# Optimization experiments

Hardware: AMD Instinct MI355X
Metric: run time of the kernel (lower is better)

## Reference

```python
import jax, jax.numpy as jnp
import numpy as np

B, T, D = 4, 2048, 1024
H, Dh = 16, 64


def setup_inputs() -> dict:
    key = jax.random.key(0)
    ks = jax.random.split(key, 5)
    # kaiming_normal_ on [H, Dh, D]: fan_in = Dh*D (torch default fan_in over dims[1:]),
    # std = sqrt(2/fan_in); exact init distribution does not affect correctness checks.
    std_qkv = float(np.sqrt(2.0 / (Dh * D)))
    std_o = float(np.sqrt(2.0 / (D * Dh)))
    return {
        "x": jax.random.normal(ks[0], (B, T, D), dtype=jnp.float32),
        "W_Q": jax.random.normal(ks[1], (H, Dh, D), dtype=jnp.float32) * std_qkv,
        "b_Q": jnp.zeros((H, Dh), dtype=jnp.float32),
        "W_K": jax.random.normal(ks[2], (H, Dh, D), dtype=jnp.float32) * std_qkv,
        "b_K": jnp.zeros((H, Dh), dtype=jnp.float32),
        "W_V": jax.random.normal(ks[3], (H, Dh, D), dtype=jnp.float32) * std_qkv,
        "b_V": jnp.zeros((H, Dh), dtype=jnp.float32),
        "W_O": jax.random.normal(ks[4], (H, D, Dh), dtype=jnp.float32) * std_o,
        "b_O": jnp.zeros((D,), dtype=jnp.float32),
    }


def reference(x, W_Q, b_Q, W_K, b_K, W_V, b_V, W_O, b_O):
    # Q/K/V: [batch, tok, heads, d_head]
    Q = jnp.einsum("btd,hkd->bthk", x, W_Q) + b_Q
    K = jnp.einsum("btd,hkd->bthk", x, W_K) + b_K
    V = jnp.einsum("btd,hkd->bthk", x, W_V) + b_V
    d_head = W_Q.shape[1]
    # scores: [batch, heads, tok_Q, tok_K]
    scores = jnp.einsum("bqhk,bshk->bhqs", Q, K) / jnp.sqrt(jnp.asarray(d_head, x.dtype))
    attn = jax.nn.softmax(scores, axis=-1)
    # out per head: [batch, tok_Q, heads, d_head]
    out_h = jnp.einsum("bhqs,bshk->bqhk", attn, V)
    # project back: [batch, tok, d_model]
    return jnp.einsum("bqhk,hdk->bqd", out_h, W_O) + b_O
```

## Files before the change

kernel.cpp:

```cpp
#include <hip/hip_runtime.h>
#include <stdint.h>


typedef __attribute__((ext_vector_type(8))) short bf16x8;
typedef __attribute__((ext_vector_type(4))) float f32x4;

#define MFMA32 __builtin_amdgcn_mfma_f32_16x16x32_bf16

#if __has_builtin(__builtin_amdgcn_exp2f)
#define EXP2(x) __builtin_amdgcn_exp2f(x)
#else
#define EXP2(x) exp2f(x)
#endif

__device__ __forceinline__ unsigned short f2bf(float f) {
  union { float f; unsigned int u; } v; v.f = f;
  unsigned int r = v.u + 0x7FFFu + ((v.u >> 16) & 1u);
  return (unsigned short)(r >> 16);
}

__device__ __forceinline__ void gl_lds16(const void* g, void* l) {
  __builtin_amdgcn_global_load_lds(
      (const __attribute__((address_space(1))) unsigned int*)g,
      (__attribute__((address_space(3))) unsigned int*)l, 16, 0, 0);
}

__device__ __forceinline__ unsigned packbf2(float lo, float hi) {
  union { float f; unsigned u; } a, b; a.f = lo; b.f = hi;
  return __builtin_amdgcn_perm(b.u, a.u, 0x07060302u);
}

__device__ __forceinline__ int rho(int r) { return (r & 3) | ((r >> 1) & 4); }

__device__ __forceinline__ void conv8(const float* __restrict__ src,
                                      unsigned short* __restrict__ dst, int i) {
  const float4* sp = (const float4*)src;
  float4 a = sp[2 * i], b = sp[2 * i + 1];
  union { unsigned short u[8]; uint4 v; } o;
  o.u[0] = f2bf(a.x); o.u[1] = f2bf(a.y); o.u[2] = f2bf(a.z); o.u[3] = f2bf(a.w);
  o.u[4] = f2bf(b.x); o.u[5] = f2bf(b.y); o.u[6] = f2bf(b.z); o.u[7] = f2bf(b.w);
  ((uint4*)dst)[i] = o.v;
}

__global__ __launch_bounds__(256) void prep_all(
    const float* __restrict__ x, const float* __restrict__ WQ,
    const float* __restrict__ WK, const float* __restrict__ WV,
    const float* __restrict__ WO, unsigned short* __restrict__ Xb,
    unsigned short* __restrict__ Wqkv, unsigned short* __restrict__ Wot) {
  const int bx = blockIdx.x, t = threadIdx.x;
  if (bx < 4096) {
    conv8(x, Xb, bx * 256 + t);
  } else if (bx < 4608) {
    conv8(WQ, Wqkv, (bx - 4096) * 256 + t);
  } else if (bx < 5120) {
    conv8(WK, Wqkv + 1048576, (bx - 4608) * 256 + t);
  } else if (bx < 5632) {
    conv8(WV, Wqkv + 2097152, (bx - 5120) * 256 + t);
  } else {
    int tid = (bx - 5632) * 256 + t;
    int h = tid >> 13, rem = tid & 8191;
    int d = rem >> 3, c = rem & 7;
    const float4* sp = (const float4*)(WO + (size_t)h * 65536 + d * 64 + c * 8);
    float4 a = sp[0], e = sp[1];
    union { unsigned short u[8]; uint4 v; } o;
    o.u[0] = f2bf(a.x); o.u[1] = f2bf(a.y); o.u[2] = f2bf(a.z); o.u[3] = f2bf(a.w);
    o.u[4] = f2bf(e.x); o.u[5] = f2bf(e.y); o.u[6] = f2bf(e.z); o.u[7] = f2bf(e.w);
    *(uint4*)(Wot + (size_t)d * 1024 + h * 64 + c * 8) = o.v;
  }
}


template <int MH, int C>
__device__ __forceinline__ void qkv_ds_a(const unsigned short* A, int wm, int quad,
                                         int l15, bf16x8 ar[4][2]) {
#pragma unroll
  for (int ii = 0; ii < 4; ++ii) {
    int ra = wm * 128 + MH * 64 + ii * 16 + l15;
    ar[ii][C] = *(const bf16x8*)(A + ra * 64 + (((C * 4 + quad) ^ (ra & 7)) * 8));
  }
}

template <int C>
__device__ __forceinline__ void qkv_ds_b(const unsigned short* B, int wn, int quad,
                                         int l15, bf16x8 br[3][2]) {
#pragma unroll
  for (int nj = 0; nj < 3; ++nj) {
    int rb = wn * 48 + nj * 16 + l15;
    br[nj][C] = *(const bf16x8*)(B + rb * 64 + (((C * 4 + quad) ^ (rb & 7)) * 8));
  }
}

template <int MH, int C>
__device__ __forceinline__ void qkv_mf(const bf16x8 ar[4][2], const bf16x8 br[3][2],
                                       f32x4 acc[8][3]) {
#pragma unroll
  for (int ii = 0; ii < 4; ++ii)
#pragma unroll
    for (int nj = 0; nj < 3; ++nj)
      acc[MH * 4 + ii][nj] =
          MFMA32(ar[ii][C], br[nj][C], acc[MH * 4 + ii][nj], 0, 0, 0);
}

#define QKV_BAR() __builtin_amdgcn_s_barrier()
#define QKV_LGKM0() asm volatile("s_waitcnt lgkmcnt(0)" ::: "memory")
#define SA_(bb, kt, u) \
  gl_lds16(Xb + (size_t)aoff[u] + (size_t)(kt) * 64, lds + (bb)*28672 + adst[u])
#define SB_(bb, kt, u) \
  gl_lds16(Wqkv + (size_t)boff[u] + (size_t)(kt) * 64, lds + (bb)*28672 + 16384 + bdst[u])

__global__ __launch_bounds__(512, 2) void gemm_qkv(
    const unsigned short* __restrict__ Xb, const unsigned short* __restrict__ Wqkv,
    const float* __restrict__ bQ, const float* __restrict__ bK,
    const float* __restrict__ bV, unsigned short* __restrict__ Qg,
    unsigned short* __restrict__ Kg, unsigned int* __restrict__ Vpg) {
  __shared__ unsigned short lds[57344];
  const int tid = threadIdx.x, lane = tid & 63, w = tid >> 6;
  const int quad = lane >> 4, l15 = lane & 15;
  const int wm = w >> 2, wn = w & 3;
  const int m0 = blockIdx.x * 256, n0 = blockIdx.y * 192;

  int aoff[4], adst[4];
#pragma unroll
  for (int u = 0; u < 4; ++u) {
    int s = u * 512 + tid, row = s >> 3;
    aoff[u] = (m0 + row) * 1024 + (((s & 7) ^ (row & 7)) * 8);
    adst[u] = s * 8;
  }
  int boff[3], bdst[3];
#pragma unroll
  for (int u = 0; u < 3; ++u) {
    int s = u * 512 + tid, row = s >> 3;
    boff[u] = (n0 + row) * 1024 + (((s & 7) ^ (row & 7)) * 8);
    bdst[u] = s * 8;
  }

  const unsigned short* A0 = lds;
  const unsigned short* B0 = lds + 16384;
  const unsigned short* A1 = lds + 28672;
  const unsigned short* B1 = lds + 45056;

  f32x4 acc[8][3];
#pragma unroll
  for (int i = 0; i < 8; ++i)
#pragma unroll
    for (int j = 0; j < 3; ++j) acc[i][j] = (f32x4){0.f, 0.f, 0.f, 0.f};
  bf16x8 ar[4][2], br[3][2];

  SA_(0, 0, 0); SA_(0, 0, 1); SA_(0, 0, 2); SA_(0, 0, 3);
  SB_(0, 0, 0); SB_(0, 0, 1); SB_(0, 0, 2);
  SB_(1, 1, 0); SB_(1, 1, 1); SB_(1, 1, 2);
  asm volatile("s_waitcnt vmcnt(3)" ::: "memory");
  QKV_BAR();

#pragma unroll 1
  for (int i = 0; i < 8; ++i) {
    const int tn = 2 * i + 2;
    const bool st = (i < 7);
    qkv_ds_a<0, 0>(A0, wm, quad, l15, ar);
    qkv_ds_b<0>(B0, wn, quad, l15, br);
    SA_(1, 2 * i + 1, 0); SA_(1, 2 * i + 1, 1);
    QKV_BAR(); QKV_LGKM0();
    __builtin_amdgcn_s_setprio(1); qkv_mf<0, 0>(ar, br, acc); __builtin_amdgcn_s_setprio(0);
    QKV_BAR();
    qkv_ds_a<0, 1>(A0, wm, quad, l15, ar);
    qkv_ds_b<1>(B0, wn, quad, l15, br);
    SA_(1, 2 * i + 1, 2); SA_(1, 2 * i + 1, 3);
    QKV_BAR(); QKV_LGKM0();
    __builtin_amdgcn_s_setprio(1); qkv_mf<0, 1>(ar, br, acc); __builtin_amdgcn_s_setprio(0);
    QKV_BAR();
    qkv_ds_a<1, 0>(A0, wm, quad, l15, ar);
    if (st) { SB_(0, tn, 0); SB_(0, tn, 1); }
    QKV_BAR(); QKV_LGKM0();
    __builtin_amdgcn_s_setprio(1); qkv_mf<1, 0>(ar, br, acc); __builtin_amdgcn_s_setprio(0);
    QKV_BAR();
    qkv_ds_a<1, 1>(A0, wm, quad, l15, ar);
    if (st) SB_(0, tn, 2);
    QKV_BAR(); QKV_LGKM0();
    __builtin_amdgcn_s_setprio(1); qkv_mf<1, 1>(ar, br, acc); __builtin_amdgcn_s_setprio(0);
    if (st) asm volatile("s_waitcnt vmcnt(3)" ::: "memory");
    else    asm volatile("s_waitcnt vmcnt(0)" ::: "memory");
    QKV_BAR();
    qkv_ds_a<0, 0>(A1, wm, quad, l15, ar);
    qkv_ds_b<0>(B1, wn, quad, l15, br);
    if (st) { SA_(0, tn, 0); SA_(0, tn, 1); }
    QKV_BAR(); QKV_LGKM0();
    __builtin_amdgcn_s_setprio(1); qkv_mf<0, 0>(ar, br, acc); __builtin_amdgcn_s_setprio(0);
    QKV_BAR();
    qkv_ds_a<0, 1>(A1, wm, quad, l15, ar);
    qkv_ds_b<1>(B1, wn, quad, l15, br);
    if (st) { SA_(0, tn, 2); SA_(0, tn, 3); }
    QKV_BAR(); QKV_LGKM0();
    __builtin_amdgcn_s_setprio(1); qkv_mf<0, 1>(ar, br, acc); __builtin_amdgcn_s_setprio(0);
    QKV_BAR();
    qkv_ds_a<1, 0>(A1, wm, quad, l15, ar);
    if (st) { SB_(1, tn + 1, 0); SB_(1, tn + 1, 1); }
    QKV_BAR(); QKV_LGKM0();
    __builtin_amdgcn_s_setprio(1); qkv_mf<1, 0>(ar, br, acc); __builtin_amdgcn_s_setprio(0);
    QKV_BAR();
    qkv_ds_a<1, 1>(A1, wm, quad, l15, ar);
    if (st) SB_(1, tn + 1, 2);
    QKV_BAR(); QKV_LGKM0();
    __builtin_amdgcn_s_setprio(1); qkv_mf<1, 1>(ar, br, acc); __builtin_amdgcn_s_setprio(0);
    asm volatile("s_waitcnt vmcnt(3)" ::: "memory");
    QKV_BAR();
  }

#pragma unroll
  for (int nj = 0; nj < 3; ++nj) {
    const int n_abs = n0 + wn * 48 + nj * 16 + l15;
    const int type = n_abs >> 10;
    const int n_in = n_abs & 1023;
    const int h = n_in >> 6, kh = n_in & 63;
    const float bv = ((type == 0) ? bQ : (type == 1) ? bK : bV)[n_in];
#pragma unroll
    for (int mi = 0; mi < 8; ++mi) {
      const int mb = m0 + wm * 128 + mi * 16 + quad * 4;
      const int b = mb >> 11, tb = mb & 2047;
      if (type == 2) {
        uint2 pk;
        pk.x = (unsigned)f2bf(acc[mi][nj][0] + bv) |
               ((unsigned)f2bf(acc[mi][nj][1] + bv) << 16);
        pk.y = (unsigned)f2bf(acc[mi][nj][2] + bv) |
               ((unsigned)f2bf(acc[mi][nj][3] + bv) << 16);
        *(uint2*)(Vpg + ((size_t)(b * 16 + h) * 64 + kh) * 1024 + (tb >> 1)) = pk;
      } else {
        unsigned short* dst =
            ((type == 0) ? Qg : Kg) + ((size_t)(b * 16 + h) * 2048 + tb) * 64 + kh;
        const float sc = (type == 0) ? 0.18033688011112042f : 1.0f;
        dst[0]   = f2bf((acc[mi][nj][0] + bv) * sc);
        dst[64]  = f2bf((acc[mi][nj][1] + bv) * sc);
        dst[128] = f2bf((acc[mi][nj][2] + bv) * sc);
        dst[192] = f2bf((acc[mi][nj][3] + bv) * sc);
      }
    }
  }
}

#undef SA_
#undef SB_
#undef QKV_BAR
#undef QKV_LGKM0

__device__ __forceinline__ void stage_kv(const unsigned short* __restrict__ Kb,
                                         const unsigned int* __restrict__ Vb,
                                         unsigned short* smem, int tid, int s0, int b) {
#pragma unroll
  for (int u = 0; u < 2; ++u) {
    int s = u * 256 + tid, row = s >> 3, g = (s & 7) ^ rho(row);
    gl_lds16(Kb + (size_t)(s0 + row) * 64 + g * 8, smem + b * 8192 + s * 8);
    gl_lds16(Vb + (size_t)row * 1024 + (s0 >> 1) + g * 4,
             smem + b * 8192 + 4096 + s * 8);
  }
}

__global__ __launch_bounds__(256, 2) void flash_attn(
    const unsigned short* __restrict__ Qg, const unsigned short* __restrict__ Kg,
    const unsigned int* __restrict__ Vpg, unsigned short* __restrict__ OH) {
  __shared__ unsigned short smem[16384];
  const int tid = threadIdx.x, lane = tid & 63, w = tid >> 6;
  const int quad = lane >> 4, l15 = lane & 15;
  const int bh = blockIdx.x, qt = blockIdx.y;

  const unsigned short* Qb = Qg + ((size_t)bh * 2048 + qt * 256) * 64;
  const unsigned short* Kb = Kg + (size_t)bh * 2048 * 64;
  const unsigned int*  Vb = Vpg + (size_t)bh * 64 * 1024;

#pragma unroll
  for (int u = 0; u < 8; ++u) {
    int s = u * 256 + tid, row = s >> 3;
    gl_lds16(Qb + row * 64 + ((s & 7) ^ (row & 7)) * 8, smem + s * 8);
  }
  __syncthreads();

  bf16x8 qf[4][2];
#pragma unroll
  for (int qi = 0; qi < 4; ++qi) {
    int row = w * 64 + qi * 16 + l15;
#pragma unroll
    for (int c = 0; c < 2; ++c)
      qf[qi][c] = *(const bf16x8*)(smem + row * 64 + (((c * 4 + quad) ^ (row & 7)) * 8));
  }
  __syncthreads();

  stage_kv(Kb, Vb, smem, tid, 0, 0);

  f32x4 o[4][4];
  float l_part[4] = {0.f, 0.f, 0.f, 0.f};
#pragma unroll
  for (int qi = 0; qi < 4; ++qi)
#pragma unroll
    for (int nj = 0; nj < 4; ++nj) o[qi][nj] = (f32x4){0.f, 0.f, 0.f, 0.f};

  for (int t = 0; t < 32; ++t) {
    __syncthreads();
    if (t < 31) stage_kv(Kb, Vb, smem, tid, (t + 1) * 64, (t + 1) & 1);
    const unsigned short* Kd = smem + (t & 1) * 8192;
    const unsigned short* Vd = Kd + 4096;

#pragma unroll
    for (int blk = 0; blk < 2; ++blk) {
      bf16x8 vb[4];
#pragma unroll
      for (int nj = 0; nj < 4; ++nj) {
        int vrow = nj * 16 + l15;
        vb[nj] = *(const bf16x8*)(Vd + vrow * 64 + (((blk * 4 + quad) ^ rho(vrow)) * 8));
      }
      union { unsigned u[4]; bf16x8 v; } pa[4];
#pragma unroll
      for (int v = 0; v < 2; ++v) {
        int krow = blk * 32 + 8 * (l15 >> 2) + 4 * v + (l15 & 3);
        const unsigned short* kr = Kd + krow * 64;
        bf16x8 ka0 = *(const bf16x8*)(kr + ((quad ^ rho(krow)) * 8));
        bf16x8 ka1 = *(const bf16x8*)(kr + (((4 + quad) ^ rho(krow)) * 8));
#pragma unroll
        for (int qi = 0; qi < 4; ++qi) {
          f32x4 S = (f32x4){0.f, 0.f, 0.f, 0.f};
          S = MFMA32(ka0, qf[qi][0], S, 0, 0, 0);
          S = MFMA32(ka1, qf[qi][1], S, 0, 0, 0);
          float e0 = EXP2(S[0]), e1 = EXP2(S[1]), e2 = EXP2(S[2]), e3 = EXP2(S[3]);
          l_part[qi] += (e0 + e1) + (e2 + e3);
          pa[qi].u[2 * v] = packbf2(e0, e1);
          pa[qi].u[2 * v + 1] = packbf2(e2, e3);
        }
      }
#pragma unroll
      for (int nj = 0; nj < 4; ++nj)
#pragma unroll
        for (int qi = 0; qi < 4; ++qi)
          o[qi][nj] = MFMA32(pa[qi].v, vb[nj], o[qi][nj], 0, 0, 0);
    }
  }

  const int b = bh >> 4, h = bh & 15;
#pragma unroll
  for (int qi = 0; qi < 4; ++qi) {
    float l = l_part[qi];
    l += __shfl_xor(l, 16);
    l += __shfl_xor(l, 32);
    float linv = 1.0f / l;
#pragma unroll
    for (int r = 0; r < 4; ++r) {
      float lr = __shfl(linv, 4 * quad + r);
      int trow = qt * 256 + w * 64 + qi * 16 + 4 * quad + r;
#pragma unroll
      for (int nj = 0; nj < 4; ++nj) {
        int col = h * 64 + nj * 16 + l15;
        OH[((size_t)b * 2048 + trow) * 1024 + col] = f2bf(o[qi][nj][r] * lr);
      }
    }
  }
}

__global__ __launch_bounds__(256) void gemm_o(
    const unsigned short* __restrict__ OHm, const unsigned short* __restrict__ Wot,
    const float* __restrict__ bO, float* __restrict__ Out) {
  __shared__ unsigned short As[128 * 64];
  __shared__ unsigned short Bs[64 * 64];
  const int tid = threadIdx.x, lane = tid & 63, w = tid >> 6;
  const int quad = lane >> 4, l15 = lane & 15;
  const int wm = w & 1, wn = w >> 1;
  const int m0 = blockIdx.x * 128, n0 = blockIdx.y * 64;
  f32x4 acc[4][2];
#pragma unroll
  for (int i = 0; i < 4; ++i)
#pragma unroll
    for (int j = 0; j < 2; ++j) acc[i][j] = (f32x4){0.f, 0.f, 0.f, 0.f};

  for (int k0 = 0; k0 < 1024; k0 += 64) {
    __syncthreads();
#pragma unroll
    for (int u = 0; u < 4; ++u) {
      int s = u * 256 + tid, row = s >> 3;
      int cl = ((s & 7) ^ (row & 7)) * 8;
      gl_lds16(OHm + (size_t)(m0 + row) * 1024 + k0 + cl, As + s * 8);
    }
#pragma unroll
    for (int u = 0; u < 2; ++u) {
      int s = u * 256 + tid, row = s >> 3;
      int cl = ((s & 7) ^ (row & 7)) * 8;
      gl_lds16(Wot + (size_t)(n0 + row) * 1024 + k0 + cl, Bs + s * 8);
    }
    __syncthreads();
    bf16x8 af[4][2], bfr[2][2];
#pragma unroll
    for (int i = 0; i < 4; ++i) {
      int ra = wm * 64 + i * 16 + l15;
#pragma unroll
      for (int c = 0; c < 2; ++c)
        af[i][c] = *(const bf16x8*)(As + ra * 64 + (((c * 4 + quad) ^ (ra & 7)) * 8));
    }
#pragma unroll
    for (int j = 0; j < 2; ++j) {
      int rb = wn * 32 + j * 16 + l15;
#pragma unroll
      for (int c = 0; c < 2; ++c)
        bfr[j][c] = *(const bf16x8*)(Bs + rb * 64 + (((c * 4 + quad) ^ (rb & 7)) * 8));
    }
#pragma unroll
    for (int mi = 0; mi < 4; ++mi)
#pragma unroll
      for (int nj = 0; nj < 2; ++nj) {
        acc[mi][nj] = MFMA32(af[mi][0], bfr[nj][0], acc[mi][nj], 0, 0, 0);
        acc[mi][nj] = MFMA32(af[mi][1], bfr[nj][1], acc[mi][nj], 0, 0, 0);
      }
  }

#pragma unroll
  for (int nj = 0; nj < 2; ++nj) {
    const int n = n0 + wn * 32 + nj * 16 + l15;
    const float bv = bO[n];
#pragma unroll
    for (int mi = 0; mi < 4; ++mi) {
      const int mb = m0 + wm * 64 + mi * 16 + quad * 4;
#pragma unroll
      for (int r = 0; r < 4; ++r)
        Out[(size_t)(mb + r) * 1024 + n] = acc[mi][nj][r] + bv;
    }
  }
}

extern "C" void kernel_launch(void* const* d_in, const int* in_sizes, int n_in,
                              void* d_out, int out_size, void* d_ws, size_t ws_size,
                              hipStream_t stream) {
  const float* x  = (const float*)d_in[0];
  const float* WQ = (const float*)d_in[1];
  const float* bQ = (const float*)d_in[2];
  const float* WK = (const float*)d_in[3];
  const float* bK = (const float*)d_in[4];
  const float* WV = (const float*)d_in[5];
  const float* bV = (const float*)d_in[6];
  const float* WO = (const float*)d_in[7];
  const float* bO = (const float*)d_in[8];
  float* out = (float*)d_out;

  char* ws = (char*)d_ws;
  unsigned short* Xb   = (unsigned short*)(ws);
  unsigned short* OH   = (unsigned short*)(ws);
  unsigned short* Wqkv = (unsigned short*)(ws + 16777216);
  unsigned short* Wot  = (unsigned short*)(ws + 23068672);
  unsigned short* Qg   = (unsigned short*)(ws + 25165824);
  unsigned short* Kg   = (unsigned short*)(ws + 41943040);
  unsigned int*   Vpg  = (unsigned int*)  (ws + 58720256);

  prep_all<<<6144, 256, 0, stream>>>(x, WQ, WK, WV, WO, Xb, Wqkv, Wot);

  dim3 g1(32, 16);
  gemm_qkv<<<g1, 512, 0, stream>>>(Xb, Wqkv, bQ, bK, bV, Qg, Kg, Vpg);
  dim3 g2(64, 8);
  flash_attn<<<g2, 256, 0, stream>>>(Qg, Kg, Vpg, OH);
  dim3 g3(64, 16);
  gemm_o<<<g3, 256, 0, stream>>>(OH, Wot, bO, out);
}
```

Baseline: 252.9 us.

## Enlarge output-projection GEMM tile to 128x128 and remap block order for locality

New measurement: 258.0 us. 1.02x slower.

```diff
diff --git a/kernel.cpp b/kernel.cpp
--- a/kernel.cpp
+++ b/kernel.cpp
@@ -69,6 +69,50 @@
   }
 }
 
+__device__ __forceinline__ void gemm_mainloop_1024(
+    const unsigned short* __restrict__ A, const unsigned short* __restrict__ B,
+    unsigned short* As, unsigned short* Bs, int m0, int n0, f32x4 acc[4][4]) {
+  const int tid = threadIdx.x;
+  const int lane = tid & 63, w = tid >> 6;
+  const int quad = lane >> 4, l15 = lane & 15;
+  const int wm = w & 1, wn = w >> 1;
+  int srow[4], scl[4];
+#pragma unroll
+  for (int u = 0; u < 4; ++u) {
+    int s = u * 256 + tid;
+    srow[u] = s >> 3;
+    scl[u] = ((s & 7) ^ ((s >> 3) & 7)) * 8;
+  }
+  for (int k0 = 0; k0 < 1024; k0 += 64) {
+    __syncthreads();
+#pragma unroll
+    for (int u = 0; u < 4; ++u) {
+      int s = u * 256 + tid;
+      gl_lds16(A + (size_t)(m0 + srow[u]) * 1024 + k0 + scl[u], As + s * 8);
+      gl_lds16(B + (size_t)(n0 + srow[u]) * 1024 + k0 + scl[u], Bs + s * 8);
+    }
+    __syncthreads();
+    bf16x8 af[4][2], bfr[4][2];
+#pragma unroll
+    for (int i = 0; i < 4; ++i) {
+      int ra = wm * 64 + i * 16 + l15;
+      int rb = wn * 64 + i * 16 + l15;
+#pragma unroll
+      for (int c = 0; c < 2; ++c) {
+        af[i][c]  = *(const bf16x8*)(As + ra * 64 + (((c * 4 + quad) ^ (ra & 7)) * 8));
+        bfr[i][c] = *(const bf16x8*)(Bs + rb * 64 + (((c * 4 + quad) ^ (rb & 7)) * 8));
+      }
+    }
+#pragma unroll
+    for (int mi = 0; mi < 4; ++mi)
+#pragma unroll
+      for (int nj = 0; nj < 4; ++nj) {
+        acc[mi][nj] = MFMA32(af[mi][0], bfr[nj][0], acc[mi][nj], 0, 0, 0);
+        acc[mi][nj] = MFMA32(af[mi][1], bfr[nj][1], acc[mi][nj], 0, 0, 0);
+      }
+  }
+}
+
 
 template <int MH, int C>
 __device__ __forceinline__ void qkv_ds_a(const unsigned short* A, int wm, int quad,
@@ -117,7 +161,9 @@
   const int tid = threadIdx.x, lane = tid & 63, w = tid >> 6;
   const int quad = lane >> 4, l15 = lane & 15;
   const int wm = w >> 2, wn = w & 3;
-  const int m0 = blockIdx.x * 256, n0 = blockIdx.y * 192;
+  const int lin = blockIdx.y * 32 + blockIdx.x;
+  const int xq = lin & 7, xc = lin >> 3;
+  const int m0 = (xq * 4 + (xc & 3)) * 256, n0 = (xc >> 2) * 192;
 
   int aoff[4], adst[4];
 #pragma unroll
@@ -355,59 +401,24 @@
     const unsigned short* __restrict__ OHm, const unsigned short* __restrict__ Wot,
     const float* __restrict__ bO, float* __restrict__ Out) {
   __shared__ unsigned short As[128 * 64];
-  __shared__ unsigned short Bs[64 * 64];
+  __shared__ unsigned short Bs[128 * 64];
   const int tid = threadIdx.x, lane = tid & 63, w = tid >> 6;
   const int quad = lane >> 4, l15 = lane & 15;
   const int wm = w & 1, wn = w >> 1;
-  const int m0 = blockIdx.x * 128, n0 = blockIdx.y * 64;
-  f32x4 acc[4][2];
+  const int lin = blockIdx.y * 64 + blockIdx.x;
+  const int xq = lin & 7, xc = lin >> 3;
+  const int m0 = (xq * 8 + (xc & 7)) * 128, n0 = (xc >> 3) * 128;
+  f32x4 acc[4][4];
 #pragma unroll
   for (int i = 0; i < 4; ++i)
 #pragma unroll
-    for (int j = 0; j < 2; ++j) acc[i][j] = (f32x4){0.f, 0.f, 0.f, 0.f};
-
-  for (int k0 = 0; k0 < 1024; k0 += 64) {
-    __syncthreads();
-#pragma unroll
-    for (int u = 0; u < 4; ++u) {
-      int s = u * 256 + tid, row = s >> 3;
-      int cl = ((s & 7) ^ (row & 7)) * 8;
-      gl_lds16(OHm + (size_t)(m0 + row) * 1024 + k0 + cl, As + s * 8);
-    }
-#pragma unroll
-    for (int u = 0; u < 2; ++u) {
-      int s = u * 256 + tid, row = s >> 3;
-      int cl = ((s & 7) ^ (row & 7)) * 8;
-      gl_lds16(Wot + (size_t)(n0 + row) * 1024 + k0 + cl, Bs + s * 8);
-    }
-    __syncthreads();
-    bf16x8 af[4][2], bfr[2][2];
-#pragma unroll
-    for (int i = 0; i < 4; ++i) {
-      int ra = wm * 64 + i * 16 + l15;
-#pragma unroll
-      for (int c = 0; c < 2; ++c)
-        af[i][c] = *(const bf16x8*)(As + ra * 64 + (((c * 4 + quad) ^ (ra & 7)) * 8));
-    }
-#pragma unroll
-    for (int j = 0; j < 2; ++j) {
-      int rb = wn * 32 + j * 16 + l15;
-#pragma unroll
-      for (int c = 0; c < 2; ++c)
-        bfr[j][c] = *(const bf16x8*)(Bs + rb * 64 + (((c * 4 + quad) ^ (rb & 7)) * 8));
-    }
-#pragma unroll
-    for (int mi = 0; mi < 4; ++mi)
-#pragma unroll
-      for (int nj = 0; nj < 2; ++nj) {
-        acc[mi][nj] = MFMA32(af[mi][0], bfr[nj][0], acc[mi][nj], 0, 0, 0);
-        acc[mi][nj] = MFMA32(af[mi][1], bfr[nj][1], acc[mi][nj], 0, 0, 0);
-      }
-  }
-
-#pragma unroll
-  for (int nj = 0; nj < 2; ++nj) {
-    const int n = n0 + wn * 32 + nj * 16 + l15;
+    for (int j = 0; j < 4; ++j) acc[i][j] = (f32x4){0.f, 0.f, 0.f, 0.f};
+
+  gemm_mainloop_1024(OHm, Wot, As, Bs, m0, n0, acc);
+
+#pragma unroll
+  for (int nj = 0; nj < 4; ++nj) {
+    const int n = n0 + wn * 64 + nj * 16 + l15;
     const float bv = bO[n];
 #pragma unroll
     for (int mi = 0; mi < 4; ++mi) {
@@ -448,6 +459,6 @@
   gemm_qkv<<<g1, 512, 0, stream>>>(Xb, Wqkv, bQ, bK, bV, Qg, Kg, Vpg);
   dim3 g2(64, 8);
   flash_attn<<<g2, 256, 0, stream>>>(Qg, Kg, Vpg, OH);
-  dim3 g3(64, 16);
+  dim3 g3(64, 8);
   gemm_o<<<g3, 256, 0, stream>>>(OH, Wot, bO, out);
 }
```
